# Kernel tuning notes

Measured on AMD Instinct MI355X. Metric: run time of the kernel, lower is better.

## Reference

```python
import jax, jax.numpy as jnp
import numpy as np

B, S, D, H = 8, 1024, 1024, 16
HD = D // H  # 64


def setup_inputs() -> dict:
    key = jax.random.key(0)
    ks = jax.random.split(key, 10)
    f32 = jnp.float32
    inp = {
        "query": jax.random.normal(ks[0], (B, S, D), f32),
        "key": jax.random.normal(ks[1], (B, S, D), f32),
        "value": jax.random.normal(ks[2], (B, S, D), f32),
        "rel": jax.random.normal(ks[3], (B, S, S), f32),
        "timestamp": jax.random.normal(ks[4], (B, S, S), f32),
        "mask": jax.random.randint(ks[5], (B, S, S), 0, 2).astype(bool),
        "l1": jnp.float32(0.3),
        "l2": jnp.float32(0.5),
        "encode_pos": 0,
        "Wq": jax.random.normal(ks[6], (D, D), f32) * 0.02,
        "bq": jnp.zeros((D,), f32),
        "Wk": jax.random.normal(ks[7], (D, D), f32) * 0.02,
        "bk": jnp.zeros((D,), f32),
        "Wv": jax.random.normal(ks[8], (D, D), f32) * 0.02,
        "bv": jnp.zeros((D,), f32),
    }
    return inp


def _proj(x, W, b):
    # nn.Linear: x @ W.T + b, then split heads -> [B, H, S, HD]
    y = x @ W.T + b
    return y.reshape(B, S, H, HD).transpose(0, 2, 1, 3)


def reference(query, key, value, rel, timestamp, mask, l1, l2, encode_pos,
              Wq, bq, Wk, bk, Wv, bv):
    # encode_pos == 0 path: QK^T + time-decay + rel-attn three-softmax blend
    q = _proj(query, Wq, bq)
    k = _proj(key, Wk, bk)
    v = _proj(value, Wv, bv)

    m = mask[:, None]                       # [B,1,S,S], broadcasts over heads
    mf = m.astype(jnp.float32)

    # rel attention: zero out where mask is False, then fill zeros with -1e5
    rel_m = rel[:, None] * mf               # [B,1,S,S]
    rel_attn = jax.nn.softmax(jnp.where(rel_m == 0, -100000.0, rel_m), axis=-1)

    inv_sqrt_d = 1.0 / np.sqrt(HD).astype(np.float32)
    scores = jnp.einsum("bhqd,bhkd->bhqk", q, k) * inv_sqrt_d
    scores = jnp.where(m, -1e32, scores)

    time_stamp = jnp.exp(-jnp.abs(timestamp[:, None]))   # [B,1,S,S]
    time_stamp = jnp.where(m, -100000.0, time_stamp)

    prob_attn = jax.nn.softmax(scores, axis=-1)          # [B,H,S,S]
    time_attn = jax.nn.softmax(time_stamp, axis=-1)      # [B,1,S,S]

    prob_attn = (1.0 - l2) * prob_attn + l2 * time_attn
    prob_attn = (1.0 - l1) * prob_attn + l1 * rel_attn
    # dropout is identity at inference

    out = jnp.einsum("bhqk,bhkd->bhqd", prob_attn, v)
    out = out.transpose(0, 2, 1, 3).reshape(B, S, D)
    return out, prob_attn
```

## Files before the change

kernel.cpp:

```cpp
#include <hip/hip_runtime.h>
#include <stdint.h>

typedef short bf16x8 __attribute__((ext_vector_type(8)));
typedef short bf16x4 __attribute__((ext_vector_type(4)));
typedef float f32x4 __attribute__((ext_vector_type(4)));
typedef unsigned short u16x4 __attribute__((ext_vector_type(4)));
typedef unsigned short u16x8 __attribute__((ext_vector_type(8)));

constexpr int NB = 8, NS = 1024, ND = 1024, NH = 16, NHD = 64;

static __device__ __forceinline__ unsigned short f2bf(float f) {
    union { float f; uint32_t u; } v; v.f = f;
    uint32_t r = (v.u + 0x7fffu + ((v.u >> 16) & 1u)) >> 16;
    return (unsigned short)r;
}

static __device__ __forceinline__ f32x4 mfma32(bf16x8 a, bf16x8 b, f32x4 c) {
    return __builtin_amdgcn_mfma_f32_16x16x32_bf16(a, b, c, 0, 0, 0);
}

static __device__ __forceinline__ f32x4 mfma16(bf16x4 a, bf16x4 b, f32x4 c) {
#if __has_builtin(__builtin_amdgcn_mfma_f32_16x16x16bf16_1k)
    return __builtin_amdgcn_mfma_f32_16x16x16bf16_1k(a, b, c, 0, 0, 0);
#elif __has_builtin(__builtin_amdgcn_mfma_f32_16x16x16_bf16)
    return __builtin_amdgcn_mfma_f32_16x16x16_bf16(a, b, c, 0, 0, 0);
#else
    asm volatile("v_mfma_f32_16x16x16_bf16 %0, %1, %2, %0\n\ts_nop 7\n\ts_nop 7"
                 : "+v"(c) : "v"(a), "v"(b));
    return c;
#endif
}

static __device__ __forceinline__ bool mask_at(const void* m, size_t idx, int ms) {
    if (ms == 4) return ((const unsigned int*)m)[idx] != 0u;
    return ((const unsigned char*)m)[idx] != 0;
}

__global__ void detect_mask(const unsigned int* __restrict__ m, int* __restrict__ flag) {
    int l = threadIdx.x;
    bool bad = false;
    for (int i = l; i < 1024; i += 64) {
        unsigned int w = m[i];
        bad |= (w > 1u && w != 0x3f800000u);
    }
    bad = (bool)__any(bad);
    if (l == 0) *flag = bad ? 1 : 4;
}

__global__ __launch_bounds__(256) void cvt_frag(const float* __restrict__ in,
                                                unsigned short* __restrict__ out, int n8) {
    int stride = gridDim.x * blockDim.x;
    for (int idx = blockIdx.x * blockDim.x + threadIdx.x; idx < n8; idx += stride) {
        const float4* p = (const float4*)in + 2 * (size_t)idx;
        float4 a = p[0], b = p[1];
        u16x8 o;
        o[0] = f2bf(a.x); o[1] = f2bf(a.y); o[2] = f2bf(a.z); o[3] = f2bf(a.w);
        o[4] = f2bf(b.x); o[5] = f2bf(b.y); o[6] = f2bf(b.z); o[7] = f2bf(b.w);
        int m = idx >> 7, c8 = idx & 127;
        int kt = c8 >> 2, sub = c8 & 3;
        int lane = (m & 15) + 16 * sub;
        size_t slot = ((size_t)(m >> 4) * 32 + kt) * 64 + lane;
        *(u16x8*)(out + slot * 8) = o;
    }
}

__global__ __launch_bounds__(256) void proj_gemm(const unsigned short* __restrict__ Af,
                                                 const unsigned short* __restrict__ Wf,
                                                 const float* __restrict__ bias,
                                                 unsigned short* __restrict__ C, int mode) {
    int l = threadIdx.x & 63, w = threadIdx.x >> 6;
    int lr = l & 15, lg = l >> 4;
    int m_base = blockIdx.x * 128 + (w >> 1) * 64;
    int n_base = blockIdx.y * 128 + (w & 1) * 64;
    int mtg0 = m_base >> 4, ntg0 = n_base >> 4;
    f32x4 acc[4][4] = {};
    for (int kt = 0; kt < 32; kt++) {
        bf16x8 af[4], bfr[4];
        #pragma unroll
        for (int mt = 0; mt < 4; mt++)
            af[mt] = *(const bf16x8*)(Af + (((size_t)(mtg0 + mt) * 32 + kt) * 64 + l) * 8);
        #pragma unroll
        for (int nt = 0; nt < 4; nt++)
            bfr[nt] = *(const bf16x8*)(Wf + (((size_t)(ntg0 + nt) * 32 + kt) * 64 + l) * 8);
        #pragma unroll
        for (int mt = 0; mt < 4; mt++) {
            #pragma unroll
            for (int nt = 0; nt < 4; nt++)
                acc[mt][nt] = mfma32(af[mt], bfr[nt], acc[mt][nt]);
        }
    }
    #pragma unroll
    for (int mt = 0; mt < 4; mt++) {
        #pragma unroll
        for (int nt = 0; nt < 4; nt++) {
            int col = n_base + nt * 16 + lr;
            int row0 = m_base + mt * 16 + lg * 4;
            float bv = bias[col];
            int b = row0 >> 10;
            int h = col >> 6;
            if (mode == 0) {
                int st = (row0 & 1023) >> 4;
                int d32 = (col & 63) >> 5;
                int sub = (col & 31) >> 3;
                int e = col & 7;
                size_t base = ((((size_t)(b * NH + h) * 64 + st) * 2 + d32) * 64) * 8;
                #pragma unroll
                for (int r = 0; r < 4; r++) {
                    int lane = lg * 4 + r + 16 * sub;
                    C[base + (size_t)lane * 8 + e] = f2bf(acc[mt][nt][r] + bv);
                }
            } else {
                int s0 = row0 & 1023;
                int tg = s0 >> 4;
                int tp = tg >> 1, half = tg & 1;
                int dd = col & 63;
                int dt = dd >> 4;
                int lane = (dd & 15) + 16 * lg;
                u16x4 pk;
                #pragma unroll
                for (int r = 0; r < 4; r++) pk[r] = f2bf(acc[mt][nt][r] + bv);
                size_t addr = ((((size_t)(b * NH + h) * 32 + tp) * 4 + dt) * 64 + lane) * 8
                              + half * 4;
                *(u16x4*)(C + addr) = pk;
            }
        }
    }
}

__global__ __launch_bounds__(256) void tr_kernel(const float* __restrict__ rel,
                                                 const float* __restrict__ ts,
                                                 const void* __restrict__ maskp,
                                                 const int* __restrict__ msflag,
                                                 const float* __restrict__ l1p,
                                                 const float* __restrict__ l2p,
                                                 float* __restrict__ TRf,
                                                 uint32_t* __restrict__ PMf) {
    __shared__ float s_tm[4], s_rm[4], s_ts[4], s_rs[4];
    __shared__ unsigned char s_nib[256];
    int row = blockIdx.x;
    int t = threadIdx.x, w = t >> 6, l = t & 63;
    int ms = *msflag;
    size_t base = (size_t)row * NS;
    float4 r4 = ((const float4*)(rel + base))[t];
    float4 t4 = ((const float4*)(ts + base))[t];
    float rr[4], tt[4];
    *(float4*)rr = r4; *(float4*)tt = t4;
    float tv[4], rv[4];
    unsigned nib = 0;
    float tmx = -3.0e38f, rmx = -3.0e38f;
    #pragma unroll
    for (int j = 0; j < 4; j++) {
        bool m = mask_at(maskp, base + t * 4 + j, ms);
        nib |= (m ? 1u : 0u) << j;
        tv[j] = m ? -100000.0f : __expf(-fabsf(tt[j]));
        float rm_ = m ? rr[j] : 0.0f;
        rv[j] = (rm_ == 0.0f) ? -100000.0f : rm_;
        tmx = fmaxf(tmx, tv[j]); rmx = fmaxf(rmx, rv[j]);
    }
    s_nib[t] = (unsigned char)nib;
    #pragma unroll
    for (int off = 1; off < 64; off <<= 1) {
        tmx = fmaxf(tmx, __shfl_xor(tmx, off));
        rmx = fmaxf(rmx, __shfl_xor(rmx, off));
    }
    if (l == 0) { s_tm[w] = tmx; s_rm[w] = rmx; }
    __syncthreads();
    tmx = fmaxf(fmaxf(s_tm[0], s_tm[1]), fmaxf(s_tm[2], s_tm[3]));
    rmx = fmaxf(fmaxf(s_rm[0], s_rm[1]), fmaxf(s_rm[2], s_rm[3]));
    float te[4], re[4], tsum = 0.f, rsum = 0.f;
    #pragma unroll
    for (int j = 0; j < 4; j++) {
        te[j] = __expf(tv[j] - tmx); tsum += te[j];
        re[j] = __expf(rv[j] - rmx); rsum += re[j];
    }
    #pragma unroll
    for (int off = 1; off < 64; off <<= 1) {
        tsum += __shfl_xor(tsum, off);
        rsum += __shfl_xor(rsum, off);
    }
    if (l == 0) { s_ts[w] = tsum; s_rs[w] = rsum; }
    __syncthreads();
    tsum = s_ts[0] + s_ts[1] + s_ts[2] + s_ts[3];
    rsum = s_rs[0] + s_rs[1] + s_rs[2] + s_rs[3];
    float l1 = *l1p, l2 = *l2p;
    float ti = ((1.0f - l1) * l2) / tsum;
    float ri = l1 / rsum;
    float4 o;
    o.x = te[0] * ti + re[0] * ri;
    o.y = te[1] * ti + re[1] * ri;
    o.z = te[2] * ti + re[2] * ri;
    o.w = te[3] * ti + re[3] * ri;
    int b = row >> 10, q = row & 1023;
    int qt = q >> 4, qr = q & 15;
    size_t slot = ((size_t)(b * 64 + qt) * 64 + (t >> 2)) * 64 + (qr + 16 * (t & 3));
    ((float4*)TRf)[slot] = o;
    if (t < 32) {
        uint32_t word = 0;
        #pragma unroll
        for (int i = 0; i < 8; i++)
            word |= ((uint32_t)s_nib[t * 8 + i]) << (i * 4);
        PMf[((size_t)(b * 64 + qt) * 16 + qr) * 32 + t] = word;
    }
}

__global__ __launch_bounds__(64, 4) void att_pv_kernel(const unsigned short* __restrict__ Qf,
                                                       const unsigned short* __restrict__ Kf,
                                                       const uint32_t* __restrict__ PMf,
                                                       const float* __restrict__ TRf,
                                                       const float* __restrict__ l1p,
                                                       const float* __restrict__ l2p,
                                                       const unsigned short* __restrict__ Vf,
                                                       float* __restrict__ probOut,
                                                       float* __restrict__ outp) {
    int bid = blockIdx.x;
    int swz = ((bid & 7) << 10) | (bid >> 3);
    int qt = swz & 63;
    int h = (swz >> 6) & 15;
    int b = swz >> 10;
    int l = threadIdx.x, lr = l & 15, lg = l >> 4;
    int q0 = qt * 16;
    int q = q0 + lr;
    size_t bh = (size_t)(b * NH + h);

    const unsigned short* qf = Qf + (((bh * 64 + qt) * 2) * 64 + l) * 8;
    bf16x8 bq0 = *(const bf16x8*)(qf);
    bf16x8 bq1 = *(const bf16x8*)(qf + 64 * 8);

    const unsigned short* kfb = Kf + ((bh * 64 * 2) * 64) * 8 + (size_t)l * 8;
    const uint32_t* pmrow = PMf + ((size_t)(b * 64 + qt) * 16 + lr) * 32;

    float sm = 0.f;
    for (int t8 = 0; t8 < 8; t8++) {
        uint32_t pmw[4];
        *(uint4*)pmw = *(const uint4*)(pmrow + t8 * 4);
        #pragma unroll
        for (int tt = 0; tt < 8; tt++) {
            int t = t8 * 8 + tt;
            const unsigned short* kp = kfb + (size_t)t * 1024;
            bf16x8 a0 = *(const bf16x8*)kp;
            bf16x8 a1 = *(const bf16x8*)(kp + 512);
            f32x4 acc = {};
            acc = mfma32(a0, bq0, acc);
            acc = mfma32(a1, bq1, acc);
            uint32_t word = pmw[tt >> 1];
            int shift = (tt & 1) * 16 + lg * 4;
            #pragma unroll
            for (int r = 0; r < 4; r++) {
                bool m = (word >> (shift + r)) & 1u;
                sm += m ? 0.0f : __expf(acc[r] * 0.125f);
            }
        }
    }
    sm += __shfl_xor(sm, 16);
    sm += __shfl_xor(sm, 32);
    float l1 = *l1p, l2 = *l2p;
    float rinv = ((1.0f - l1) * (1.0f - l2)) / sm;

    float* po = probOut + bh * NS * NS + (size_t)q * NS;
    const float4* trf = (const float4*)TRf + ((size_t)(b * 64 + qt) * 64) * 64 + l;
    const unsigned short* vf = Vf + (bh * 32 * 4 * 64) * 8 + (size_t)l * 8;
    f32x4 acc2[4] = {};
    for (int tq = 0; tq < 8; tq++) {
        uint32_t pmw[4];
        *(uint4*)pmw = *(const uint4*)(pmrow + tq * 4);
        #pragma unroll
        for (int tpi = 0; tpi < 4; tpi++) {
            int tp = tq * 4 + tpi;
            bf16x4 pf0, pf1;
            #pragma unroll
            for (int hf = 0; hf < 2; hf++) {
                int t = tp * 2 + hf;
                const unsigned short* kp = kfb + (size_t)t * 1024;
                bf16x8 a0 = *(const bf16x8*)kp;
                bf16x8 a1 = *(const bf16x8*)(kp + 512);
                f32x4 acc = {};
                acc = mfma32(a0, bq0, acc);
                acc = mfma32(a1, bq1, acc);
                uint32_t word = pmw[tpi];
                int shift = hf * 16 + lg * 4;
                float4 tr4 = ((const float4*)trf)[(size_t)t * 64];
                float4 o;
                float e0 = ((word >> (shift + 0)) & 1u) ? 0.f : __expf(acc[0] * 0.125f);
                float e1 = ((word >> (shift + 1)) & 1u) ? 0.f : __expf(acc[1] * 0.125f);
                float e2 = ((word >> (shift + 2)) & 1u) ? 0.f : __expf(acc[2] * 0.125f);
                float e3 = ((word >> (shift + 3)) & 1u) ? 0.f : __expf(acc[3] * 0.125f);
                o.x = e0 * rinv + tr4.x;
                o.y = e1 * rinv + tr4.y;
                o.z = e2 * rinv + tr4.z;
                o.w = e3 * rinv + tr4.w;
                *(float4*)(po + t * 16 + lg * 4) = o;
                bf16x4 pk;
                pk[0] = (short)f2bf(o.x); pk[1] = (short)f2bf(o.y);
                pk[2] = (short)f2bf(o.z); pk[3] = (short)f2bf(o.w);
                if (hf == 0) pf0 = pk; else pf1 = pk;
            }
            #pragma unroll
            for (int dt = 0; dt < 4; dt++) {
                bf16x8 vv = *(const bf16x8*)(vf + (size_t)(tp * 4 + dt) * 512);
                bf16x4 v0 = __builtin_shufflevector(vv, vv, 0, 1, 2, 3);
                bf16x4 v1 = __builtin_shufflevector(vv, vv, 4, 5, 6, 7);
                acc2[dt] = mfma16(v0, pf0, acc2[dt]);
                acc2[dt] = mfma16(v1, pf1, acc2[dt]);
            }
        }
    }
    float* orow = outp + ((size_t)b * NS + q) * ND + h * NHD + lg * 4;
    #pragma unroll
    for (int dt = 0; dt < 4; dt++) {
        float4 ov;
        ov.x = acc2[dt][0]; ov.y = acc2[dt][1]; ov.z = acc2[dt][2]; ov.w = acc2[dt][3];
        *(float4*)(orow + dt * 16) = ov;
    }
}

extern "C" void kernel_launch(void* const* d_in, const int* in_sizes, int n_in,
                              void* d_out, int out_size, void* d_ws, size_t ws_size,
                              hipStream_t stream) {
    const float* query = (const float*)d_in[0];
    const float* key   = (const float*)d_in[1];
    const float* value = (const float*)d_in[2];
    const float* rel   = (const float*)d_in[3];
    const float* ts    = (const float*)d_in[4];
    const void*  mask  = d_in[5];
    const float* l1p   = (const float*)d_in[6];
    const float* l2p   = (const float*)d_in[7];
    const float* Wq = (const float*)d_in[9];
    const float* bq = (const float*)d_in[10];
    const float* Wk = (const float*)d_in[11];
    const float* bk = (const float*)d_in[12];
    const float* Wv = (const float*)d_in[13];
    const float* bv = (const float*)d_in[14];

    char* ws = (char*)d_ws;
    const size_t SZ = (size_t)NB * NS * ND * 2;
    unsigned short* Qf  = (unsigned short*)(ws);
    unsigned short* Kf  = (unsigned short*)(ws + SZ);
    unsigned short* Vf  = (unsigned short*)(ws + 2 * SZ);
    unsigned short* Afq = (unsigned short*)(ws + 3 * SZ);
    unsigned short* Afk = (unsigned short*)(ws + 4 * SZ);
    unsigned short* Afv = (unsigned short*)(ws + 5 * SZ);
    unsigned short* Wfq = (unsigned short*)(ws + 6 * SZ);
    unsigned short* Wfk = (unsigned short*)(ws + 6 * SZ + 2u * 1024 * 1024);
    unsigned short* Wfv = (unsigned short*)(ws + 6 * SZ + 4u * 1024 * 1024);
    int* msflag         = (int*)(ws + 6 * SZ + 6u * 1024 * 1024);
    uint32_t* PMf       = (uint32_t*)(ws + 6 * SZ + 8u * 1024 * 1024);
    float* TRf = (float*)(ws + 3 * SZ);

    detect_mask<<<1, 64, 0, stream>>>((const unsigned int*)mask, msflag);

    const int nX8 = NB * NS * ND / 8;
    const int nW8 = 1024 * 1024 / 8;
    cvt_frag<<<1024, 256, 0, stream>>>(query, Afq, nX8);
    cvt_frag<<<1024, 256, 0, stream>>>(key,   Afk, nX8);
    cvt_frag<<<1024, 256, 0, stream>>>(value, Afv, nX8);
    cvt_frag<<<256, 256, 0, stream>>>(Wq, Wfq, nW8);
    cvt_frag<<<256, 256, 0, stream>>>(Wk, Wfk, nW8);
    cvt_frag<<<256, 256, 0, stream>>>(Wv, Wfv, nW8);

    dim3 pg(64, 8);
    proj_gemm<<<pg, 256, 0, stream>>>(Afq, Wfq, bq, Qf, 0);
    proj_gemm<<<pg, 256, 0, stream>>>(Afk, Wfk, bk, Kf, 0);
    proj_gemm<<<pg, 256, 0, stream>>>(Afv, Wfv, bv, Vf, 1);

    tr_kernel<<<NB * NS, 256, 0, stream>>>(rel, ts, mask, msflag, l1p, l2p, TRf, PMf);

    float* outp = (float*)d_out;
    float* probOut = outp + (size_t)NB * NS * ND;
    att_pv_kernel<<<NB * NH * (NS / 16), 64, 0, stream>>>(Qf, Kf, PMf, TRf, l1p, l2p, Vf,
                                                          probOut, outp);
}
```

Before: 515.5 us.

## Cache first-half exp scores in registers, reorder block mapping, use nontemporal stores

The pass that computes the row sum now keeps the bf16-rounded exp values for the first half of the key tiles in registers. The second pass reuses them instead of recomputing QK^T and exp, which removes about half of the recomputation. The block index mapping changes so that batch is the fastest-varying index. Probability and output writes now use nontemporal stores. The 32-entry register cache raises VGPR pressure and may spill or lower occupancy under launch_bounds(64,4), and reusing bf16-rounded exp values slightly lowers the precision of the probability output.

Measured after the change: 1.432 ms. +177.9%, slower.

```diff
diff --git a/kernel.cpp b/kernel.cpp
--- a/kernel.cpp
+++ b/kernel.cpp
@@ -13,6 +13,11 @@
     union { float f; uint32_t u; } v; v.f = f;
     uint32_t r = (v.u + 0x7fffu + ((v.u >> 16) & 1u)) >> 16;
     return (unsigned short)r;
+}
+
+static __device__ __forceinline__ float bf2f(unsigned short b) {
+    union { uint32_t u; float f; } v; v.u = ((uint32_t)b) << 16;
+    return v.f;
 }
 
 static __device__ __forceinline__ f32x4 mfma32(bf16x8 a, bf16x8 b, f32x4 c) {
@@ -213,10 +218,10 @@
                                                        float* __restrict__ probOut,
                                                        float* __restrict__ outp) {
     int bid = blockIdx.x;
-    int swz = ((bid & 7) << 10) | (bid >> 3);
-    int qt = swz & 63;
-    int h = (swz >> 6) & 15;
-    int b = swz >> 10;
+    int b = bid & 7;
+    int idx = bid >> 3;
+    int h = idx & 15;
+    int qt = idx >> 4;
     int l = threadIdx.x, lr = l & 15, lg = l >> 4;
     int q0 = qt * 16;
     int q = q0 + lr;
@@ -230,7 +235,35 @@
     const uint32_t* pmrow = PMf + ((size_t)(b * 64 + qt) * 16 + lr) * 32;
 
     float sm = 0.f;
-    for (int t8 = 0; t8 < 8; t8++) {
+    bf16x4 p0[32];
+    #pragma unroll
+    for (int t8 = 0; t8 < 4; t8++) {
+        uint32_t pmw[4];
+        *(uint4*)pmw = *(const uint4*)(pmrow + t8 * 4);
+        #pragma unroll
+        for (int tt = 0; tt < 8; tt++) {
+            int t = t8 * 8 + tt;
+            const unsigned short* kp = kfb + (size_t)t * 1024;
+            bf16x8 a0 = *(const bf16x8*)kp;
+            bf16x8 a1 = *(const bf16x8*)(kp + 512);
+            f32x4 acc = {};
+            acc = mfma32(a0, bq0, acc);
+            acc = mfma32(a1, bq1, acc);
+            uint32_t word = pmw[tt >> 1];
+            int shift = (tt & 1) * 16 + lg * 4;
+            bf16x4 pk;
+            #pragma unroll
+            for (int r = 0; r < 4; r++) {
+                bool m = (word >> (shift + r)) & 1u;
+                float e = m ? 0.0f : __expf(acc[r] * 0.125f);
+                sm += e;
+                pk[r] = (short)f2bf(e);
+            }
+            p0[t] = pk;
+        }
+    }
+    #pragma unroll
+    for (int t8 = 4; t8 < 8; t8++) {
         uint32_t pmw[4];
         *(uint4*)pmw = *(const uint4*)(pmrow + t8 * 4);
         #pragma unroll
@@ -260,7 +293,37 @@
     const float4* trf = (const float4*)TRf + ((size_t)(b * 64 + qt) * 64) * 64 + l;
     const unsigned short* vf = Vf + (bh * 32 * 4 * 64) * 8 + (size_t)l * 8;
     f32x4 acc2[4] = {};
-    for (int tq = 0; tq < 8; tq++) {
+
+    #pragma unroll
+    for (int tp = 0; tp < 16; tp++) {
+        bf16x4 pf0, pf1;
+        #pragma unroll
+        for (int hf = 0; hf < 2; hf++) {
+            int t = tp * 2 + hf;
+            bf16x4 eb = p0[t];
+            float4 tr4 = trf[(size_t)t * 64];
+            f32x4 o;
+            o[0] = bf2f((unsigned short)eb[0]) * rinv + tr4.x;
+            o[1] = bf2f((unsigned short)eb[1]) * rinv + tr4.y;
+            o[2] = bf2f((unsigned short)eb[2]) * rinv + tr4.z;
+            o[3] = bf2f((unsigned short)eb[3]) * rinv + tr4.w;
+            __builtin_nontemporal_store(o, (f32x4*)(po + t * 16 + lg * 4));
+            bf16x4 pk;
+            pk[0] = (short)f2bf(o[0]); pk[1] = (short)f2bf(o[1]);
+            pk[2] = (short)f2bf(o[2]); pk[3] = (short)f2bf(o[3]);
+            if (hf == 0) pf0 = pk; else pf1 = pk;
+        }
+        #pragma unroll
+        for (int dt = 0; dt < 4; dt++) {
+            bf16x8 vv = *(const bf16x8*)(vf + (size_t)(tp * 4 + dt) * 512);
+            bf16x4 v0 = __builtin_shufflevector(vv, vv, 0, 1, 2, 3);
+            bf16x4 v1 = __builtin_shufflevector(vv, vv, 4, 5, 6, 7);
+            acc2[dt] = mfma16(v0, pf0, acc2[dt]);
+            acc2[dt] = mfma16(v1, pf1, acc2[dt]);
+        }
+    }
+    #pragma unroll
+    for (int tq = 4; tq < 8; tq++) {
         uint32_t pmw[4];
         *(uint4*)pmw = *(const uint4*)(pmrow + tq * 4);
         #pragma unroll
@@ -278,20 +341,20 @@
                 acc = mfma32(a1, bq1, acc);
                 uint32_t word = pmw[tpi];
                 int shift = hf * 16 + lg * 4;
-                float4 tr4 = ((const float4*)trf)[(size_t)t * 64];
-                float4 o;
+                float4 tr4 = trf[(size_t)t * 64];
                 float e0 = ((word >> (shift + 0)) & 1u) ? 0.f : __expf(acc[0] * 0.125f);
                 float e1 = ((word >> (shift + 1)) & 1u) ? 0.f : __expf(acc[1] * 0.125f);
                 float e2 = ((word >> (shift + 2)) & 1u) ? 0.f : __expf(acc[2] * 0.125f);
                 float e3 = ((word >> (shift + 3)) & 1u) ? 0.f : __expf(acc[3] * 0.125f);
-                o.x = e0 * rinv + tr4.x;
-                o.y = e1 * rinv + tr4.y;
-                o.z = e2 * rinv + tr4.z;
-                o.w = e3 * rinv + tr4.w;
-                *(float4*)(po + t * 16 + lg * 4) = o;
+                f32x4 o;
+                o[0] = e0 * rinv + tr4.x;
+                o[1] = e1 * rinv + tr4.y;
+                o[2] = e2 * rinv + tr4.z;
+                o[3] = e3 * rinv + tr4.w;
+                __builtin_nontemporal_store(o, (f32x4*)(po + t * 16 + lg * 4));
                 bf16x4 pk;
-                pk[0] = (short)f2bf(o.x); pk[1] = (short)f2bf(o.y);
-                pk[2] = (short)f2bf(o.z); pk[3] = (short)f2bf(o.w);
+                pk[0] = (short)f2bf(o[0]); pk[1] = (short)f2bf(o[1]);
+                pk[2] = (short)f2bf(o[2]); pk[3] = (short)f2bf(o[3]);
                 if (hf == 0) pf0 = pk; else pf1 = pk;
             }
             #pragma unroll
@@ -307,9 +370,8 @@
     float* orow = outp + ((size_t)b * NS + q) * ND + h * NHD + lg * 4;
     #pragma unroll
     for (int dt = 0; dt < 4; dt++) {
-        float4 ov;
-        ov.x = acc2[dt][0]; ov.y = acc2[dt][1]; ov.z = acc2[dt][2]; ov.w = acc2[dt][3];
-        *(float4*)(orow + dt * 16) = ov;
+        f32x4 ov = acc2[dt];
+        __builtin_nontemporal_store(ov, (f32x4*)(orow + dt * 16));
     }
 }
 
```

## Store time/rel blend term in fp16 and retile attention block order

Applied to the files above, without the earlier changes.

The precomputed time+rel softmax blend (TR) is now written and read as fp16 instead of fp32, halving its write traffic in tr_kernel and its read traffic in att_pv_kernel. The block-index mapping in att_pv_kernel is also reworked so concurrently scheduled blocks cover a 4-head by 16-query-tile patch per batch, which is meant to improve L2 reuse of TR, K and V across heads. The fp16 storage adds rounding error to the probability output.

New measurement: 524.1 us. Within noise of the previous version (+1.7%).

```diff
diff --git a/kernel.cpp b/kernel.cpp
--- a/kernel.cpp
+++ b/kernel.cpp
@@ -1,4 +1,5 @@
 #include <hip/hip_runtime.h>
+#include <hip/hip_fp16.h>
 #include <stdint.h>
 
 typedef short bf16x8 __attribute__((ext_vector_type(8)));
@@ -13,6 +14,13 @@
     union { float f; uint32_t u; } v; v.f = f;
     uint32_t r = (v.u + 0x7fffu + ((v.u >> 16) & 1u)) >> 16;
     return (unsigned short)r;
+}
+
+static __device__ __forceinline__ unsigned short f2h(float f) {
+    return __half_as_ushort(__float2half(f));
+}
+static __device__ __forceinline__ float h2f(unsigned short h) {
+    return __half2float(__ushort_as_half(h));
 }
 
 static __device__ __forceinline__ f32x4 mfma32(bf16x8 a, bf16x8 b, f32x4 c) {
@@ -133,7 +141,7 @@
                                                  const int* __restrict__ msflag,
                                                  const float* __restrict__ l1p,
                                                  const float* __restrict__ l2p,
-                                                 float* __restrict__ TRf,
+                                                 unsigned short* __restrict__ TRh,
                                                  uint32_t* __restrict__ PMf) {
     __shared__ float s_tm[4], s_rm[4], s_ts[4], s_rs[4];
     __shared__ unsigned char s_nib[256];
@@ -185,15 +193,15 @@
     float l1 = *l1p, l2 = *l2p;
     float ti = ((1.0f - l1) * l2) / tsum;
     float ri = l1 / rsum;
-    float4 o;
-    o.x = te[0] * ti + re[0] * ri;
-    o.y = te[1] * ti + re[1] * ri;
-    o.z = te[2] * ti + re[2] * ri;
-    o.w = te[3] * ti + re[3] * ri;
+    u16x4 oh;
+    oh[0] = f2h(te[0] * ti + re[0] * ri);
+    oh[1] = f2h(te[1] * ti + re[1] * ri);
+    oh[2] = f2h(te[2] * ti + re[2] * ri);
+    oh[3] = f2h(te[3] * ti + re[3] * ri);
     int b = row >> 10, q = row & 1023;
     int qt = q >> 4, qr = q & 15;
     size_t slot = ((size_t)(b * 64 + qt) * 64 + (t >> 2)) * 64 + (qr + 16 * (t & 3));
-    ((float4*)TRf)[slot] = o;
+    ((u16x4*)TRh)[slot] = oh;
     if (t < 32) {
         uint32_t word = 0;
         #pragma unroll
@@ -206,17 +214,17 @@
 __global__ __launch_bounds__(64, 4) void att_pv_kernel(const unsigned short* __restrict__ Qf,
                                                        const unsigned short* __restrict__ Kf,
                                                        const uint32_t* __restrict__ PMf,
-                                                       const float* __restrict__ TRf,
+                                                       const unsigned short* __restrict__ TRh,
                                                        const float* __restrict__ l1p,
                                                        const float* __restrict__ l2p,
                                                        const unsigned short* __restrict__ Vf,
                                                        float* __restrict__ probOut,
                                                        float* __restrict__ outp) {
     int bid = blockIdx.x;
-    int swz = ((bid & 7) << 10) | (bid >> 3);
-    int qt = swz & 63;
-    int h = (swz >> 6) & 15;
-    int b = swz >> 10;
+    int b = bid & 7;
+    int i = bid >> 3;
+    int qt = ((i >> 6) & 3) * 16 + (i & 15);
+    int h  = (i >> 8) * 4 + ((i >> 4) & 3);
     int l = threadIdx.x, lr = l & 15, lg = l >> 4;
     int q0 = qt * 16;
     int q = q0 + lr;
@@ -257,7 +265,7 @@
     float rinv = ((1.0f - l1) * (1.0f - l2)) / sm;
 
     float* po = probOut + bh * NS * NS + (size_t)q * NS;
-    const float4* trf = (const float4*)TRf + ((size_t)(b * 64 + qt) * 64) * 64 + l;
+    const u16x4* trh = (const u16x4*)TRh + ((size_t)(b * 64 + qt) * 64) * 64 + l;
     const unsigned short* vf = Vf + (bh * 32 * 4 * 64) * 8 + (size_t)l * 8;
     f32x4 acc2[4] = {};
     for (int tq = 0; tq < 8; tq++) {
@@ -278,16 +286,16 @@
                 acc = mfma32(a1, bq1, acc);
                 uint32_t word = pmw[tpi];
                 int shift = hf * 16 + lg * 4;
-                float4 tr4 = ((const float4*)trf)[(size_t)t * 64];
+                u16x4 tr4 = trh[(size_t)t * 64];
                 float4 o;
                 float e0 = ((word >> (shift + 0)) & 1u) ? 0.f : __expf(acc[0] * 0.125f);
                 float e1 = ((word >> (shift + 1)) & 1u) ? 0.f : __expf(acc[1] * 0.125f);
                 float e2 = ((word >> (shift + 2)) & 1u) ? 0.f : __expf(acc[2] * 0.125f);
                 float e3 = ((word >> (shift + 3)) & 1u) ? 0.f : __expf(acc[3] * 0.125f);
-                o.x = e0 * rinv + tr4.x;
-                o.y = e1 * rinv + tr4.y;
-                o.z = e2 * rinv + tr4.z;
-                o.w = e3 * rinv + tr4.w;
+                o.x = e0 * rinv + h2f(tr4[0]);
+                o.y = e1 * rinv + h2f(tr4[1]);
+                o.z = e2 * rinv + h2f(tr4[2]);
+                o.w = e3 * rinv + h2f(tr4[3]);
                 *(float4*)(po + t * 16 + lg * 4) = o;
                 bf16x4 pk;
                 pk[0] = (short)f2bf(o.x); pk[1] = (short)f2bf(o.y);
@@ -344,7 +352,7 @@
     unsigned short* Wfv = (unsigned short*)(ws + 6 * SZ + 4u * 1024 * 1024);
     int* msflag         = (int*)(ws + 6 * SZ + 6u * 1024 * 1024);
     uint32_t* PMf       = (uint32_t*)(ws + 6 * SZ + 8u * 1024 * 1024);
-    float* TRf = (float*)(ws + 3 * SZ);
+    unsigned short* TRh = (unsigned short*)(ws + 3 * SZ);
 
     detect_mask<<<1, 64, 0, stream>>>((const unsigned int*)mask, msflag);
 
@@ -362,10 +370,10 @@
     proj_gemm<<<pg, 256, 0, stream>>>(Afk, Wfk, bk, Kf, 0);
     proj_gemm<<<pg, 256, 0, stream>>>(Afv, Wfv, bv, Vf, 1);
 
-    tr_kernel<<<NB * NS, 256, 0, stream>>>(rel, ts, mask, msflag, l1p, l2p, TRf, PMf);
+    tr_kernel<<<NB * NS, 256, 0, stream>>>(rel, ts, mask, msflag, l1p, l2p, TRh, PMf);
 
     float* outp = (float*)d_out;
     float* probOut = outp + (size_t)NB * NS * ND;
-    att_pv_kernel<<<NB * NH * (NS / 16), 64, 0, stream>>>(Qf, Kf, PMf, TRf, l1p, l2p, Vf,
+    att_pv_kernel<<<NB * NH * (NS / 16), 64, 0, stream>>>(Qf, Kf, PMf, TRh, l1p, l2p, Vf,
                                                           probOut, outp);
 }
```
